# Optimization experiments

Hardware: AMD Instinct MI355X
Metric: run time of the kernel (lower is better)

The kernel has to match this reference:

```python
import jax, jax.numpy as jnp
import numpy as np

D_MODEL, D_STATE, DT_RANK = 1024, 16, 64
BATCH, SEQLEN = 2, 4096

def setup_inputs() -> dict:
    key = jax.random.key(0)
    ks = jax.random.split(key, 6)
    x = jax.random.normal(ks[0], (BATCH, SEQLEN, D_MODEL), dtype=jnp.float32)
    # A = arange(1..N) repeated per channel; A_log = log(A)
    A = jnp.tile(jnp.arange(1, D_STATE + 1, dtype=jnp.float32)[None, :], (D_MODEL, 1))
    A_log = jnp.log(A)
    D_param = jnp.ones((D_MODEL,), dtype=jnp.float32)
    dt_init_std = DT_RANK ** -0.5
    dt_proj_w = jax.random.uniform(ks[1], (D_MODEL, DT_RANK), minval=-dt_init_std, maxval=dt_init_std, dtype=jnp.float32)
    dt = jnp.exp(jax.random.uniform(ks[2], (D_MODEL,)) * (np.log(0.1) - np.log(0.001)) + np.log(0.001))
    dt_proj_b = dt + jnp.log(-jnp.expm1(-dt))
    x_to_dtBC_w = jax.random.normal(ks[3], (DT_RANK + 2 * D_STATE, D_MODEL), dtype=jnp.float32) * (D_MODEL ** -0.5)
    return {"x": x, "A_log": A_log, "D_param": D_param, "dt_proj_w": dt_proj_w, "dt_proj_b": dt_proj_b, "x_to_dtBC_w": x_to_dtBC_w}

def reference(x, A_log, D_param, dt_proj_w, dt_proj_b, x_to_dtBC_w):
    # x: (B,L,D)
    dtBC = jnp.einsum('bld,ed->ble', x, x_to_dtBC_w)            # (B,L,dt_rank+2N)
    dt_in = dtBC[..., :DT_RANK]
    B_in = dtBC[..., DT_RANK:DT_RANK + D_STATE]                  # (B,L,N)
    C_in = dtBC[..., DT_RANK + D_STATE:]                         # (B,L,N)
    dt = jax.nn.softplus(jnp.einsum('blr,dr->bld', dt_in, dt_proj_w) + dt_proj_b)  # (B,L,D)
    A = -jnp.exp(A_log)                                          # (D,N)
    dA = jnp.exp(dt[..., None] * A[None, None])                  # (B,L,D,N)
    dB = dt[..., None] * B_in[:, :, None, :]                     # (B,L,D,N)
    dBx = dB * x[..., None]                                      # (B,L,D,N)

    def step(h, inputs):
        dA_t, dBx_t, C_t = inputs                                # (B,D,N),(B,D,N),(B,N)
        h = dA_t * h + dBx_t
        y_t = jnp.einsum('bdn,bn->bd', h, C_t)
        return h, y_t

    h0 = jnp.zeros((x.shape[0], D_MODEL, D_STATE), dtype=x.dtype)
    xs = (jnp.swapaxes(dA, 0, 1), jnp.swapaxes(dBx, 0, 1), jnp.swapaxes(C_in, 0, 1))
    _, ys = jax.lax.scan(step, h0, xs)                           # (L,B,D)
    y = jnp.swapaxes(ys, 0, 1) + x * D_param[None, None, :]
    return y
```

## Files before the change

kernel.cpp:

```cpp
#include <hip/hip_runtime.h>

#define D_MODEL 1024
#define D_STATE 16
#define DT_RANK 64
#define BATCH 2
#define SEQLEN 4096
#define NROWS (BATCH * SEQLEN)
#define E_DIM 96
#define CH 32
#define NCH (SEQLEN / CH)

typedef short bf16x8 __attribute__((ext_vector_type(8)));
typedef float f32x4 __attribute__((ext_vector_type(4)));

__global__ __launch_bounds__(256)
void k_prep(const float* __restrict__ Wx, const float* __restrict__ W2,
            unsigned short* __restrict__ Wxbf, float* __restrict__ W2T) {
  const int bid = blockIdx.x;
  if (bid < 384) {
    const int idx = bid * 256 + threadIdx.x;
    unsigned int u = __float_as_uint(Wx[idx]);
    u = (u + 0x7fffu + ((u >> 16) & 1u)) >> 16;
    Wxbf[idx] = (unsigned short)u;
  } else {
    const int idx = (bid - 384) * 256 + threadIdx.x;
    const int r = idx >> 10;
    const int d = idx & 1023;
    W2T[idx] = W2[(size_t)d * DT_RANK + r];
  }
}

#define KSPLIT 4
#define KSEG (D_MODEL / KSPLIT)

__global__ __launch_bounds__(256)
void k_gemm1(const float* __restrict__ x, const unsigned short* __restrict__ Wxbf,
             float* __restrict__ parts) {
  __shared__ unsigned short sXb[64][72];
  __shared__ unsigned short sWb[96][72];
  const int tid = threadIdx.x;
  const int lane = tid & 63, w = tid >> 6;
  const int r = lane & 15, kq = lane >> 4;
  const int m0 = blockIdx.x * 64;
  const int ks0 = blockIdx.y * KSEG;

  f32x4 acc[6];
  #pragma unroll
  for (int j = 0; j < 6; ++j) acc[j] = (f32x4){0.f, 0.f, 0.f, 0.f};

  for (int kt = 0; kt < KSEG; kt += 64) {
    #pragma unroll
    for (int s = 0; s < 4; ++s) {
      const int f = s * 256 + tid;
      const int row = f >> 4, k4 = f & 15;
      const float4 v = *reinterpret_cast<const float4*>(
          &x[(size_t)(m0 + row) * D_MODEL + ks0 + kt + k4 * 4]);
      unsigned int u0, u1;
      asm("v_cvt_pk_bf16_f32 %0, %1, %2" : "=v"(u0) : "v"(v.x), "v"(v.y));
      asm("v_cvt_pk_bf16_f32 %0, %1, %2" : "=v"(u1) : "v"(v.z), "v"(v.w));
      *reinterpret_cast<uint2*>(&sXb[row][k4 * 4]) = make_uint2(u0, u1);
    }
    #pragma unroll
    for (int s = 0; s < 3; ++s) {
      const int f = s * 256 + tid;
      const int e = f >> 3, k8 = f & 7;
      *reinterpret_cast<uint4*>(&sWb[e][k8 * 8]) =
          *reinterpret_cast<const uint4*>(
              &Wxbf[(size_t)e * D_MODEL + ks0 + kt + k8 * 8]);
    }
    __syncthreads();
    #pragma unroll
    for (int ks = 0; ks < 2; ++ks) {
      const bf16x8 af = *reinterpret_cast<const bf16x8*>(
          &sXb[w * 16 + r][ks * 32 + kq * 8]);
      #pragma unroll
      for (int j = 0; j < 6; ++j) {
        const bf16x8 bf = *reinterpret_cast<const bf16x8*>(
            &sWb[j * 16 + r][ks * 32 + kq * 8]);
        acc[j] = __builtin_amdgcn_mfma_f32_16x16x32_bf16(af, bf, acc[j], 0, 0, 0);
      }
    }
    __syncthreads();
  }
  float* op = parts + (size_t)blockIdx.y * (NROWS * E_DIM);
  #pragma unroll
  for (int j = 0; j < 6; ++j)
    #pragma unroll
    for (int i = 0; i < 4; ++i)
      op[(size_t)(m0 + w * 16 + kq * 4 + i) * E_DIM + j * 16 + r] = acc[j][i];
}

__global__ __launch_bounds__(256)
void k_reduce(const float* __restrict__ parts, float* __restrict__ dtBC) {
  const int i = blockIdx.x * 256 + threadIdx.x;
  const float4* p = reinterpret_cast<const float4*>(parts);
  float4 a = p[i];
  #pragma unroll
  for (int s = 1; s < KSPLIT; ++s) {
    const float4 b = p[(size_t)s * (NROWS * E_DIM / 4) + i];
    a.x += b.x; a.y += b.y; a.z += b.z; a.w += b.w;
  }
  reinterpret_cast<float4*>(dtBC)[i] = a;
}

#define G2_ROWS 32

__global__ __launch_bounds__(256)
void k_dt(const float* __restrict__ dtBC, const float* __restrict__ W2T,
          const float* __restrict__ b2, float* __restrict__ dt) {
  const int d = blockIdx.x * 256 + threadIdx.x;
  const int m0 = blockIdx.y * G2_ROWS;
  const float bias = b2[d];
  float acc[G2_ROWS];
  #pragma unroll
  for (int i = 0; i < G2_ROWS; ++i) acc[i] = bias;

  for (int r = 0; r < DT_RANK; ++r) {
    const float w = W2T[(size_t)r * D_MODEL + d];
    #pragma unroll
    for (int i = 0; i < G2_ROWS; ++i)
      acc[i] = fmaf(dtBC[(size_t)(m0 + i) * E_DIM + r], w, acc[i]);
  }
  #pragma unroll
  for (int i = 0; i < G2_ROWS; ++i) {
    const float a = acc[i];
    const float sp = (a > 15.f) ? a : __logf(1.f + __expf(a));
    dt[(size_t)(m0 + i) * D_MODEL + d] = sp;
  }
}

__global__ __launch_bounds__(256)
void k_scanA(const float* __restrict__ dt, const float* __restrict__ x,
             const float* __restrict__ dtBC, const float* __restrict__ A_log,
             float* __restrict__ P, float* __restrict__ U) {
  const int d = blockIdx.x * 256 + threadIdx.x;
  const int c = blockIdx.y;
  const int b = blockIdx.z;
  const int t0 = c * CH;

  __shared__ float sB[CH][D_STATE];
  for (int idx = threadIdx.x; idx < CH * D_STATE; idx += 256) {
    const int t = idx >> 4, n = idx & 15;
    sB[t][n] = dtBC[(size_t)(b * SEQLEN + t0 + t) * E_DIM + DT_RANK + n];
  }
  __syncthreads();

  float Ar[D_STATE];
  #pragma unroll
  for (int q = 0; q < 4; ++q) {
    const float4 v = *reinterpret_cast<const float4*>(
        &A_log[(size_t)d * D_STATE + q * 4]);
    Ar[q * 4 + 0] = -__expf(v.x); Ar[q * 4 + 1] = -__expf(v.y);
    Ar[q * 4 + 2] = -__expf(v.z); Ar[q * 4 + 3] = -__expf(v.w);
  }

  float Pr[D_STATE], Ur[D_STATE];
  #pragma unroll
  for (int n = 0; n < D_STATE; ++n) { Pr[n] = 1.f; Ur[n] = 0.f; }

  const float* dtp = dt + (size_t)(b * SEQLEN + t0) * D_MODEL + d;
  const float* xp  = x  + (size_t)(b * SEQLEN + t0) * D_MODEL + d;

  float dtv = dtp[0];
  float xv  = xp[0];
  for (int t = 0; t < CH; ++t) {
    float dtn = 0.f, xn = 0.f;
    if (t + 1 < CH) {
      dtn = dtp[(size_t)(t + 1) * D_MODEL];
      xn  = xp[(size_t)(t + 1) * D_MODEL];
    }
    const float z = dtv * xv;
    #pragma unroll
    for (int n = 0; n < D_STATE; ++n) {
      const float e = __expf(dtv * Ar[n]);
      Ur[n] = fmaf(e, Ur[n], z * sB[t][n]);
      Pr[n] *= e;
    }
    dtv = dtn; xv = xn;
  }
  const size_t base = (size_t)(b * NCH + c) * (D_STATE * D_MODEL) + d;
  #pragma unroll
  for (int n = 0; n < D_STATE; ++n) {
    P[base + (size_t)n * D_MODEL] = Pr[n];
    U[base + (size_t)n * D_MODEL] = Ur[n];
  }
}

__global__ __launch_bounds__(256)
void k_scanB(const float* __restrict__ P, const float* __restrict__ U,
             float* __restrict__ hst) {
  const int idx = blockIdx.x * 256 + threadIdx.x;
  const int b = idx >> 14;
  const int nd = idx & 16383;
  float h = 0.f;
  for (int c0 = 0; c0 < NCH; c0 += 8) {
    float p[8], u[8];
    #pragma unroll
    for (int i = 0; i < 8; ++i) {
      const size_t off = (size_t)(b * NCH + c0 + i) * (D_STATE * D_MODEL) + nd;
      p[i] = P[off]; u[i] = U[off];
    }
    #pragma unroll
    for (int i = 0; i < 8; ++i) {
      const size_t off = (size_t)(b * NCH + c0 + i) * (D_STATE * D_MODEL) + nd;
      hst[off] = h;
      h = fmaf(p[i], h, u[i]);
    }
  }
}

__global__ __launch_bounds__(256)
void k_scanC(const float* __restrict__ dt, const float* __restrict__ x,
             const float* __restrict__ dtBC, const float* __restrict__ A_log,
             const float* __restrict__ Dp, const float* __restrict__ hst,
             float* __restrict__ y) {
  const int d = blockIdx.x * 256 + threadIdx.x;
  const int c = blockIdx.y;
  const int b = blockIdx.z;
  const int t0 = c * CH;

  __shared__ float sBC[CH][2 * D_STATE];
  for (int idx = threadIdx.x; idx < CH * 2 * D_STATE; idx += 256) {
    const int t = idx >> 5, j = idx & 31;
    sBC[t][j] = dtBC[(size_t)(b * SEQLEN + t0 + t) * E_DIM + DT_RANK + j];
  }
  __syncthreads();

  float Ar[D_STATE];
  #pragma unroll
  for (int q = 0; q < 4; ++q) {
    const float4 v = *reinterpret_cast<const float4*>(
        &A_log[(size_t)d * D_STATE + q * 4]);
    Ar[q * 4 + 0] = -__expf(v.x); Ar[q * 4 + 1] = -__expf(v.y);
    Ar[q * 4 + 2] = -__expf(v.z); Ar[q * 4 + 3] = -__expf(v.w);
  }
  const float Dv = Dp[d];

  float h[D_STATE];
  const size_t hbase = (size_t)(b * NCH + c) * (D_STATE * D_MODEL) + d;
  #pragma unroll
  for (int n = 0; n < D_STATE; ++n) h[n] = hst[hbase + (size_t)n * D_MODEL];

  const float* dtp = dt + (size_t)(b * SEQLEN + t0) * D_MODEL + d;
  const float* xp  = x  + (size_t)(b * SEQLEN + t0) * D_MODEL + d;
  float* yp        = y  + (size_t)(b * SEQLEN + t0) * D_MODEL + d;

  float dtv = dtp[0];
  float xv  = xp[0];
  for (int t = 0; t < CH; ++t) {
    float dtn = 0.f, xn = 0.f;
    if (t + 1 < CH) {
      dtn = dtp[(size_t)(t + 1) * D_MODEL];
      xn  = xp[(size_t)(t + 1) * D_MODEL];
    }
    const float z = dtv * xv;
    float acc = 0.f;
    #pragma unroll
    for (int n = 0; n < D_STATE; ++n) {
      const float e = __expf(dtv * Ar[n]);
      h[n] = fmaf(e, h[n], z * sBC[t][n]);
      acc = fmaf(h[n], sBC[t][D_STATE + n], acc);
    }
    yp[(size_t)t * D_MODEL] = fmaf(xv, Dv, acc);
    dtv = dtn; xv = xn;
  }
}

extern "C" void kernel_launch(void* const* d_in, const int* in_sizes, int n_in,
                              void* d_out, int out_size, void* d_ws, size_t ws_size,
                              hipStream_t stream) {
  const float* x     = (const float*)d_in[0];
  const float* A_log = (const float*)d_in[1];
  const float* Dp    = (const float*)d_in[2];
  const float* W2    = (const float*)d_in[3];
  const float* b2    = (const float*)d_in[4];
  const float* Wx    = (const float*)d_in[5];
  float* out = (float*)d_out;

  float* ws = (float*)d_ws;
  float* dtBC  = ws;
  float* dtbuf = ws +   786432;
  float* P     = ws +  9175040;
  float* U     = ws + 13369344;
  float* hst   = ws + 17563648;
  float* parts = P;
  unsigned short* Wxbf = (unsigned short*)hst;
  float* W2T           = hst + 49152;

  hipLaunchKernelGGL(k_prep, dim3(640), dim3(256), 0, stream, Wx, W2, Wxbf, W2T);
  hipLaunchKernelGGL(k_gemm1, dim3(NROWS / 64, KSPLIT), dim3(256), 0, stream,
                     x, Wxbf, parts);
  hipLaunchKernelGGL(k_reduce, dim3(NROWS * E_DIM / 4 / 256), dim3(256), 0,
                     stream, parts, dtBC);
  hipLaunchKernelGGL(k_dt, dim3(D_MODEL / 256, NROWS / G2_ROWS), dim3(256), 0,
                     stream, dtBC, W2T, b2, dtbuf);
  hipLaunchKernelGGL(k_scanA, dim3(D_MODEL / 256, NCH, BATCH), dim3(256),
                     0, stream, dtbuf, x, dtBC, A_log, P, U);
  hipLaunchKernelGGL(k_scanB, dim3((BATCH * D_STATE * D_MODEL) / 256),
                     dim3(256), 0, stream, P, U, hst);
  hipLaunchKernelGGL(k_scanC, dim3(D_MODEL / 256, NCH, BATCH), dim3(256),
                     0, stream, dtbuf, x, dtBC, A_log, Dp, hst, out);
}
```

Before: 213.6 us.

## Compute dt projection with bf16 MFMA instead of scalar FP32 FMAs

Replaces the scalar FP32 dt projection kernel with a bf16 MFMA kernel. The reduce kernel now also writes a bf16 copy of the dt_in slice, and the prep kernel converts W2 to bf16 instead of transposing it. This is meant to cut the FP32 FMA and redundant global-load cost of the 8192x1024x64 GEMM, at the cost of bf16 rounding of dt_in and W2 before the softplus.

```diff
diff --git a/kernel.cpp b/kernel.cpp
--- a/kernel.cpp
+++ b/kernel.cpp
@@ -15,7 +15,7 @@
 
 __global__ __launch_bounds__(256)
 void k_prep(const float* __restrict__ Wx, const float* __restrict__ W2,
-            unsigned short* __restrict__ Wxbf, float* __restrict__ W2T) {
+            unsigned short* __restrict__ Wxbf, unsigned short* __restrict__ W2bf) {
   const int bid = blockIdx.x;
   if (bid < 384) {
     const int idx = bid * 256 + threadIdx.x;
@@ -24,9 +24,9 @@
     Wxbf[idx] = (unsigned short)u;
   } else {
     const int idx = (bid - 384) * 256 + threadIdx.x;
-    const int r = idx >> 10;
-    const int d = idx & 1023;
-    W2T[idx] = W2[(size_t)d * DT_RANK + r];
+    unsigned int u = __float_as_uint(W2[idx]);
+    u = (u + 0x7fffu + ((u >> 16) & 1u)) >> 16;
+    W2bf[idx] = (unsigned short)u;
   }
 }
 
@@ -91,7 +91,8 @@
 }
 
 __global__ __launch_bounds__(256)
-void k_reduce(const float* __restrict__ parts, float* __restrict__ dtBC) {
+void k_reduce(const float* __restrict__ parts, float* __restrict__ dtBC,
+              unsigned short* __restrict__ dt_in_bf) {
   const int i = blockIdx.x * 256 + threadIdx.x;
   const float4* p = reinterpret_cast<const float4*>(parts);
   float4 a = p[i];
@@ -101,31 +102,51 @@
     a.x += b.x; a.y += b.y; a.z += b.z; a.w += b.w;
   }
   reinterpret_cast<float4*>(dtBC)[i] = a;
-}
-
-#define G2_ROWS 32
-
-__global__ __launch_bounds__(256)
-void k_dt(const float* __restrict__ dtBC, const float* __restrict__ W2T,
-          const float* __restrict__ b2, float* __restrict__ dt) {
-  const int d = blockIdx.x * 256 + threadIdx.x;
-  const int m0 = blockIdx.y * G2_ROWS;
-  const float bias = b2[d];
-  float acc[G2_ROWS];
-  #pragma unroll
-  for (int i = 0; i < G2_ROWS; ++i) acc[i] = bias;
-
-  for (int r = 0; r < DT_RANK; ++r) {
-    const float w = W2T[(size_t)r * D_MODEL + d];
-    #pragma unroll
-    for (int i = 0; i < G2_ROWS; ++i)
-      acc[i] = fmaf(dtBC[(size_t)(m0 + i) * E_DIM + r], w, acc[i]);
-  }
-  #pragma unroll
-  for (int i = 0; i < G2_ROWS; ++i) {
-    const float a = acc[i];
-    const float sp = (a > 15.f) ? a : __logf(1.f + __expf(a));
-    dt[(size_t)(m0 + i) * D_MODEL + d] = sp;
+  const int m = i / 24;
+  const int f4 = i - m * 24;
+  if (f4 < 16) {
+    unsigned int u0, u1;
+    asm("v_cvt_pk_bf16_f32 %0, %1, %2" : "=v"(u0) : "v"(a.x), "v"(a.y));
+    asm("v_cvt_pk_bf16_f32 %0, %1, %2" : "=v"(u1) : "v"(a.z), "v"(a.w));
+    *reinterpret_cast<uint2*>(&dt_in_bf[(size_t)m * DT_RANK + f4 * 4]) =
+        make_uint2(u0, u1);
+  }
+}
+
+__global__ __launch_bounds__(256)
+void k_dtm(const unsigned short* __restrict__ dt_in_bf,
+           const unsigned short* __restrict__ W2bf,
+           const float* __restrict__ b2, float* __restrict__ dt) {
+  const int tid = threadIdx.x;
+  const int lane = tid & 63, w = tid >> 6;
+  const int r = lane & 15, kq = lane >> 4;
+  const int m0 = blockIdx.x * 64 + w * 16;
+  const int d0 = blockIdx.y * 64;
+
+  f32x4 acc[4];
+  #pragma unroll
+  for (int j = 0; j < 4; ++j) acc[j] = (f32x4){0.f, 0.f, 0.f, 0.f};
+
+  #pragma unroll
+  for (int ks = 0; ks < 2; ++ks) {
+    const bf16x8 af = *reinterpret_cast<const bf16x8*>(
+        &dt_in_bf[(size_t)(m0 + r) * DT_RANK + ks * 32 + kq * 8]);
+    #pragma unroll
+    for (int j = 0; j < 4; ++j) {
+      const bf16x8 bf = *reinterpret_cast<const bf16x8*>(
+          &W2bf[(size_t)(d0 + j * 16 + r) * DT_RANK + ks * 32 + kq * 8]);
+      acc[j] = __builtin_amdgcn_mfma_f32_16x16x32_bf16(af, bf, acc[j], 0, 0, 0);
+    }
+  }
+  #pragma unroll
+  for (int j = 0; j < 4; ++j) {
+    const float bias = b2[d0 + j * 16 + r];
+    #pragma unroll
+    for (int i = 0; i < 4; ++i) {
+      const float a = acc[j][i] + bias;
+      const float sp = (a > 15.f) ? a : __logf(1.f + __expf(a));
+      dt[(size_t)(m0 + kq * 4 + i) * D_MODEL + d0 + j * 16 + r] = sp;
+    }
   }
 }
 
@@ -284,16 +305,17 @@
   float* U     = ws + 13369344;
   float* hst   = ws + 17563648;
   float* parts = P;
-  unsigned short* Wxbf = (unsigned short*)hst;
-  float* W2T           = hst + 49152;
-
-  hipLaunchKernelGGL(k_prep, dim3(640), dim3(256), 0, stream, Wx, W2, Wxbf, W2T);
+  unsigned short* Wxbf     = (unsigned short*)hst;
+  unsigned short* W2bf     = (unsigned short*)(hst + 49152);
+  unsigned short* dt_in_bf = (unsigned short*)(hst + 82944);
+
+  hipLaunchKernelGGL(k_prep, dim3(640), dim3(256), 0, stream, Wx, W2, Wxbf, W2bf);
   hipLaunchKernelGGL(k_gemm1, dim3(NROWS / 64, KSPLIT), dim3(256), 0, stream,
                      x, Wxbf, parts);
   hipLaunchKernelGGL(k_reduce, dim3(NROWS * E_DIM / 4 / 256), dim3(256), 0,
-                     stream, parts, dtBC);
-  hipLaunchKernelGGL(k_dt, dim3(D_MODEL / 256, NROWS / G2_ROWS), dim3(256), 0,
-                     stream, dtBC, W2T, b2, dtbuf);
+                     stream, parts, dtBC, dt_in_bf);
+  hipLaunchKernelGGL(k_dtm, dim3(NROWS / 64, D_MODEL / 64), dim3(256), 0,
+                     stream, dt_in_bf, W2bf, b2, dtbuf);
   hipLaunchKernelGGL(k_scanA, dim3(D_MODEL / 256, NCH, BATCH), dim3(256),
                      0, stream, dtbuf, x, dtBC, A_log, P, U);
   hipLaunchKernelGGL(k_scanB, dim3((BATCH * D_STATE * D_MODEL) / 256),
```

Measured after the change: 188.7 us. -11.7%, faster.
